# Optimization experiments

Measured on AMD Instinct MI355X. Metric: run time of the kernel, lower is better.

Reference implementation:

```python
import jax, jax.numpy as jnp
import numpy as np
import math

NH = 12  # num_attention_heads (multiple of 4 required by pattern dispatch)


def _forward(Input, hidden_states, attention_mask, Wq, bq, Wk, bk, Wv, bv, Wo, bo, L):
    b, n, _, H = Input.shape
    hd = H // NH
    G = NH // 4  # heads per criss-cross pattern
    # boolean-mask gather of valid (head, tail) entity pairs, row-major like torch
    bi, ri, ci = jnp.nonzero(attention_mask > 0, size=L)
    x = Input[bi, ri, ci]            # [L, H] keys/values source
    xq = hidden_states[bi, ri, ci]   # [L, H] query source
    q = (xq @ Wq + bq).reshape(L, NH, hd)
    k = (x @ Wk + bk).reshape(L, NH, hd)
    v = (x @ Wv + bv).reshape(L, NH, hd)
    ar = jnp.arange(n)
    # per-pattern criss-cross masks for query position (b, r, c), each [L, n]
    m0 = attention_mask[bi, ri, :] * (ar[None, :] != ci[:, None])  # row r, exclude self col c
    m1 = attention_mask[bi, :, ci] * (ar[None, :] != ri[:, None])  # col c, exclude self row r
    m2 = attention_mask[bi, :, ri]                                  # col r (no self exclusion)
    m3 = attention_mask[bi, ci, :]                                  # row c (no self exclusion)
    adds = jnp.stack([(1.0 - m) * -10000.0 for m in (m0, m1, m2, m3)], axis=1)  # [L, 4, n]
    # scatter per-pattern head groups into zero grid, then criss-cross gather
    k_gs, v_gs = [], []
    for p in range(4):
        sk = jnp.zeros((b, n, n, G, hd), k.dtype).at[bi, ri, ci].set(k[:, p::4])
        sv = jnp.zeros((b, n, n, G, hd), v.dtype).at[bi, ri, ci].set(v[:, p::4])
        if p == 0:
            gk, gv = sk[bi, ri], sv[bi, ri]          # element [l,k] = grid[b, r, k]
        elif p == 1:
            gk, gv = sk[bi, :, ci], sv[bi, :, ci]    # grid[b, k, c]
        elif p == 2:
            gk, gv = sk[bi, :, ri], sv[bi, :, ri]    # grid[b, k, r]
        else:
            gk, gv = sk[bi, ci], sv[bi, ci]          # grid[b, c, k]
        k_gs.append(gk)
        v_gs.append(gv)
    kg = jnp.stack(k_gs, axis=1)  # [L, 4, n, G, hd]
    vg = jnp.stack(v_gs, axis=1)
    # head h = 4*g + p (k[:, p::4] picks heads p, p+4, p+8)
    kg = kg.transpose(0, 3, 1, 2, 4).reshape(L, NH, n, hd)
    vg = vg.transpose(0, 3, 1, 2, 4).reshape(L, NH, n, hd)
    amask = jnp.broadcast_to(adds[:, None, :, :], (L, G, 4, n)).reshape(L, NH, n)
    # prepend self key/value; NOTE: original code uses additive bias +1.0 (ones) for the self slot
    kf = jnp.concatenate([k[:, :, None, :], kg], axis=2)   # [L, NH, n+1, hd]
    vf = jnp.concatenate([v[:, :, None, :], vg], axis=2)
    amask = jnp.concatenate([jnp.ones((L, NH, 1), amask.dtype), amask], axis=-1)
    scores = jnp.einsum('lhd,lhkd->lhk', q, kf) / math.sqrt(hd) + amask
    probs = jax.nn.softmax(scores, axis=-1)  # dropout is identity in eval
    ctx = jnp.einsum('lhk,lhkd->lhd', probs, vf).reshape(L, H)
    return ctx @ Wo + bo


def setup_inputs() -> dict:
    key = jax.random.key(0)
    ks = jax.random.split(key, 8)
    b, n, H = 2, 40, 768
    Input = jax.random.normal(ks[0], (b, n, n, H), jnp.float32)
    hidden_states = jax.random.normal(ks[1], (b, n, n, H), jnp.float32)
    # all valid entity pairs except self pairs -> deterministic L
    attention_mask = (jnp.ones((b, n, n)) - jnp.eye(n)[None]).astype(jnp.float32)
    L = int(b * n * (n - 1))  # 3120
    std = 0.02
    Wq = std * jax.random.normal(ks[2], (H, H), jnp.float32)
    Wk = std * jax.random.normal(ks[3], (H, H), jnp.float32)
    Wv = std * jax.random.normal(ks[4], (H, H), jnp.float32)
    Wo = std * jax.random.normal(ks[5], (H, H), jnp.float32)
    bq = jnp.zeros((H,), jnp.float32)
    bk = jnp.zeros((H,), jnp.float32)
    bv = jnp.zeros((H,), jnp.float32)
    bo = jnp.zeros((H,), jnp.float32)
    return {"Input": Input, "hidden_states": hidden_states, "attention_mask": attention_mask,
            "Wq": Wq, "bq": bq, "Wk": Wk, "bk": bk, "Wv": Wv, "bv": bv, "Wo": Wo, "bo": bo, "L": L}


def reference(Input, hidden_states, attention_mask, Wq, bq, Wk, bk, Wv, bv, Wo, bo, L):
    return _forward(Input, hidden_states, attention_mask, Wq, bq, Wk, bk, Wv, bv, Wo, bo, L)
```

## Files before the change

### kernel.cpp

```cpp
#include <hip/hip_runtime.h>
#include <hip/hip_bf16.h>
#include <math.h>

#define NHEADS 12

typedef __attribute__((ext_vector_type(4))) float f32x4;
typedef __attribute__((ext_vector_type(8))) short bf16x8;

__device__ __forceinline__ unsigned short f2bf(float x) {
  __hip_bfloat16 h = __float2bfloat16(x);
  return *reinterpret_cast<unsigned short*>(&h);
}
__device__ __forceinline__ float bf2f(unsigned short u) {
  union { unsigned int i; float f; } c; c.i = ((unsigned int)u) << 16; return c.f;
}

__global__ __launch_bounds__(256) void prep(const float* __restrict__ mask, int total,
                                            int* __restrict__ pos2l, int* __restrict__ lidx,
                                            const float* __restrict__ bk, const float* __restrict__ bv,
                                            float* __restrict__ bkv,
                                            const float* __restrict__ W0, const float* __restrict__ W1,
                                            const float* __restrict__ W2, const float* __restrict__ W3,
                                            unsigned short* __restrict__ T0, unsigned short* __restrict__ T1,
                                            unsigned short* __restrict__ T2, unsigned short* __restrict__ T3,
                                            int H) {
  int nt32 = H / 32;
  int nw = nt32 * nt32 * 4;
  int bx = blockIdx.x;
  int t = threadIdx.x;
  if (bx < nw) {
    __shared__ float tile[32][33];
    int z = bx / (nt32 * nt32);
    int rem = bx - z * nt32 * nt32;
    int byy = rem / nt32;
    int bxx = rem - byy * nt32;
    const float* W = (z == 0) ? W0 : (z == 1) ? W1 : (z == 2) ? W2 : W3;
    unsigned short* T = (z == 0) ? T0 : (z == 1) ? T1 : (z == 2) ? T2 : T3;
    int k0 = byy * 32, n0 = bxx * 32;
    int kk = t >> 3, n4 = (t & 7) * 4;
    float4 v = *reinterpret_cast<const float4*>(W + (size_t)(k0 + kk) * H + n0 + n4);
    tile[n4 + 0][kk] = v.x; tile[n4 + 1][kk] = v.y; tile[n4 + 2][kk] = v.z; tile[n4 + 3][kk] = v.w;
    __syncthreads();
    int nn2 = t >> 3, k4 = (t & 7) * 4;
#pragma unroll
    for (int e = 0; e < 4; ++e)
      T[(size_t)(n0 + nn2) * H + k0 + k4 + e] = f2bf(tile[nn2][k4 + e]);
  } else {
    __shared__ int cnt[256];
    for (int i = t; i < H; i += 256) { bkv[i] = bk[i]; bkv[H + i] = bv[i]; }
    int per = (total + 255) >> 8;
    int begin = t * per;
    int end = begin + per; if (end > total) end = total;
    if (begin > total) begin = total;
    int c = 0;
    for (int i = begin; i < end; ++i) c += (mask[i] > 0.f) ? 1 : 0;
    cnt[t] = c;
    __syncthreads();
    for (int off = 1; off < 256; off <<= 1) {
      int vv = (t >= off) ? cnt[t - off] : 0;
      __syncthreads();
      cnt[t] += vv;
      __syncthreads();
    }
    int excl = cnt[t] - c;
    for (int i = begin; i < end; ++i) {
      if (mask[i] > 0.f) { pos2l[i] = excl; lidx[excl] = i; ++excl; }
      else pos2l[i] = -1;
    }
  }
}

__global__ __launch_bounds__(256) void gatherconv(const float* __restrict__ hidden,
                                                  const float* __restrict__ input,
                                                  const int* __restrict__ lidx,
                                                  unsigned short* __restrict__ Aq,
                                                  unsigned short* __restrict__ Akv,
                                                  int L, int H) {
  int i = blockIdx.x * 256 + threadIdx.x;
  int per = H / 8;
  if (i >= L * per) return;
  int row = i / per;
  int sub = (i - row * per) * 8;
  size_t src = (size_t)lidx[row] * H + sub;
  size_t dst = (size_t)row * H + sub;
  {
    float4 a = *reinterpret_cast<const float4*>(hidden + src);
    float4 b = *reinterpret_cast<const float4*>(hidden + src + 4);
    bf16x8 st;
    st[0]=f2bf(a.x); st[1]=f2bf(a.y); st[2]=f2bf(a.z); st[3]=f2bf(a.w);
    st[4]=f2bf(b.x); st[5]=f2bf(b.y); st[6]=f2bf(b.z); st[7]=f2bf(b.w);
    *reinterpret_cast<bf16x8*>(Aq + dst) = st;
  }
  {
    float4 a = *reinterpret_cast<const float4*>(input + src);
    float4 b = *reinterpret_cast<const float4*>(input + src + 4);
    bf16x8 st;
    st[0]=f2bf(a.x); st[1]=f2bf(a.y); st[2]=f2bf(a.z); st[3]=f2bf(a.w);
    st[4]=f2bf(b.x); st[5]=f2bf(b.y); st[6]=f2bf(b.z); st[7]=f2bf(b.w);
    *reinterpret_cast<bf16x8*>(Akv + dst) = st;
  }
}

#define GBM 128
#define GBN 64
#define GBK 64

template <bool OUT_BF16>
__device__ __forceinline__ void gemm_core(const unsigned short* __restrict__ A,
                                          const unsigned short* __restrict__ Bt,
                                          const float* __restrict__ bias,
                                          void* __restrict__ C,
                                          int M, int N, int K, int m0, int n0,
                                          unsigned short* sA, unsigned short* sB) {
  int tid = threadIdx.x;
  int wid = tid >> 6, lane = tid & 63;
  int wm = wid >> 1, wn = wid & 1;
  int lr = lane & 15, lq = lane >> 4;
  f32x4 acc[4][2] = {};

  auto STAGE = [&](int buf, int k0) {
#pragma unroll
    for (int r = 0; r < 4; ++r) {
      int c = (r * 4 + wid) * 64 + lane;
      int row = c >> 3, sl = c & 7;
      int sg = sl ^ (row & 7);
      const unsigned short* g = A + (size_t)(m0 + row) * K + k0 + sg * 8;
      __builtin_amdgcn_global_load_lds((const __attribute__((address_space(1))) unsigned int*)g,
                                       (__attribute__((address_space(3))) unsigned int*)(sA + buf * (GBM * GBK) + (r * 4 + wid) * 512),
                                       16, 0, 0);
    }
#pragma unroll
    for (int r = 0; r < 2; ++r) {
      int c = (r * 4 + wid) * 64 + lane;
      int row = c >> 3, sl = c & 7;
      int sg = sl ^ (row & 7);
      const unsigned short* g = Bt + (size_t)(n0 + row) * K + k0 + sg * 8;
      __builtin_amdgcn_global_load_lds((const __attribute__((address_space(1))) unsigned int*)g,
                                       (__attribute__((address_space(3))) unsigned int*)(sB + buf * (GBN * GBK) + (r * 4 + wid) * 512),
                                       16, 0, 0);
    }
  };

  const int nt = K / GBK;
  STAGE(0, 0);
  int cur = 0;
  for (int t = 0; t < nt; ++t) {
    __syncthreads();
    if (t + 1 < nt) STAGE(cur ^ 1, (t + 1) * GBK);
    const unsigned short* pA = sA + cur * (GBM * GBK);
    const unsigned short* pB = sB + cur * (GBN * GBK);
#pragma unroll
    for (int ks = 0; ks < 2; ++ks) {
      bf16x8 af[4], bfr[2];
#pragma unroll
      for (int i = 0; i < 4; ++i) {
        int row = wm * 64 + i * 16 + lr;
        int slot = (ks * 4 + lq) ^ (row & 7);
        af[i] = *reinterpret_cast<const bf16x8*>(pA + row * 64 + slot * 8);
      }
#pragma unroll
      for (int j = 0; j < 2; ++j) {
        int rn = wn * 32 + j * 16 + lr;
        int slot = (ks * 4 + lq) ^ (rn & 7);
        bfr[j] = *reinterpret_cast<const bf16x8*>(pB + rn * 64 + slot * 8);
      }
#pragma unroll
      for (int i = 0; i < 4; ++i)
#pragma unroll
        for (int j = 0; j < 2; ++j)
          acc[i][j] = __builtin_amdgcn_mfma_f32_16x16x32_bf16(af[i], bfr[j], acc[i][j], 0, 0, 0);
    }
    cur ^= 1;
  }

#pragma unroll
  for (int i = 0; i < 4; ++i) {
#pragma unroll
    for (int j = 0; j < 2; ++j) {
      int gcol = n0 + wn * 32 + j * 16 + lr;
      float bv = bias[gcol];
      int rbase = m0 + wm * 64 + i * 16 + lq * 4;
#pragma unroll
      for (int r = 0; r < 4; ++r) {
        int gm = rbase + r;
        if (gm >= M) continue;
        float val = acc[i][j][r] + bv;
        if (OUT_BF16) ((unsigned short*)C)[(size_t)gm * N + gcol] = f2bf(val);
        else          ((float*)C)[(size_t)gm * N + gcol] = val;
      }
    }
  }
}

__global__ __launch_bounds__(256) void gemm_qkv(const unsigned short* __restrict__ Aq,
                                                const unsigned short* __restrict__ Akv,
                                                const unsigned short* __restrict__ Wqt,
                                                const unsigned short* __restrict__ Wkvt,
                                                const float* __restrict__ bq,
                                                const float* __restrict__ bkv,
                                                unsigned short* __restrict__ Cq,
                                                unsigned short* __restrict__ Ckv,
                                                int M, int K, int H) {
  __shared__ unsigned short sA[2 * GBM * GBK];
  __shared__ unsigned short sB[2 * GBN * GBK];
  int nq = H / GBN;
  int bx = blockIdx.x;
  int m0 = blockIdx.y * GBM;
  if (bx < nq)
    gemm_core<true>(Aq, Wqt, bq, Cq, M, H, K, m0, bx * GBN, sA, sB);
  else
    gemm_core<true>(Akv, Wkvt, bkv, Ckv, M, 2 * H, K, m0, (bx - nq) * GBN, sA, sB);
}

__global__ __launch_bounds__(256) void gemm_out(const unsigned short* __restrict__ A,
                                                const unsigned short* __restrict__ Bt,
                                                const float* __restrict__ bias,
                                                float* __restrict__ C,
                                                int M, int N, int K) {
  __shared__ unsigned short sA[2 * GBM * GBK];
  __shared__ unsigned short sB[2 * GBN * GBK];
  gemm_core<false>(A, Bt, bias, C, M, N, K, blockIdx.y * GBM, blockIdx.x * GBN, sA, sB);
}

__global__ __launch_bounds__(128) void attn3(const unsigned short* __restrict__ qb,
                                             const unsigned short* __restrict__ KVb,
                                             const float* __restrict__ mask,
                                             const int* __restrict__ pos2l,
                                             unsigned short* __restrict__ ctx,
                                             int n, int H) {
  __shared__ unsigned short Ks[40 * 72];
  __shared__ unsigned short Vs[40 * 72];
  __shared__ float S[40][42];
  __shared__ float mrow[40];
  __shared__ int qlist[40];

  int bx = blockIdx.x;
  int r0 = bx % n;
  int h3 = (bx / n) % 3;
  int p = (bx / (3 * n)) % 4;
  int bi = bx / (12 * n);
  int h = p + 4 * h3;
  int nn = n * n;
  bool rowkeys = (p == 0 || p == 3);
  bool rowq = (p == 0 || p == 2);
  bool excl = (p < 2);
  int t = threadIdx.x;
  int H2 = 2 * H;

  if (t < 80) {
    int half = t / 40, j = t % 40;
    int keypos = rowkeys ? (r0 * n + j) : (j * n + r0);
    int l2 = pos2l[bi * nn + keypos];
    unsigned short* dst = (half ? Vs : Ks) + j * 72;
    if (l2 >= 0) {
      const unsigned short* src = KVb + (size_t)l2 * H2 + half * H + h * 64;
#pragma unroll
      for (int e8 = 0; e8 < 8; ++e8)
        *reinterpret_cast<bf16x8*>(dst + e8 * 8) = *reinterpret_cast<const bf16x8*>(src + e8 * 8);
    } else {
      bf16x8 z = {};
#pragma unroll
      for (int e8 = 0; e8 < 8; ++e8) *reinterpret_cast<bf16x8*>(dst + e8 * 8) = z;
    }
  }
  if (t < 40) {
    mrow[t] = rowkeys ? mask[bi * nn + r0 * n + t] : mask[bi * nn + t * n + r0];
    int qpos = rowq ? (r0 * n + t) : (t * n + r0);
    qlist[t] = pos2l[bi * nn + qpos];
  }
  __syncthreads();

  int c = t % 40;
  int role = t / 40;
  int lq = (t < 80) ? qlist[c] : -1;

  if (lq >= 0) {
    float qf[64];
    const unsigned short* qp = qb + (size_t)lq * H + h * 64;
#pragma unroll
    for (int e8 = 0; e8 < 8; ++e8) {
      bf16x8 t8 = *reinterpret_cast<const bf16x8*>(qp + e8 * 8);
#pragma unroll
      for (int e = 0; e < 8; ++e) qf[e8 * 8 + e] = bf2f((unsigned short)t8[e]);
    }
    int j0 = role * 20;
#pragma unroll 2
    for (int j = j0; j < j0 + 20; ++j) {
      float acc = 0.f;
#pragma unroll
      for (int e8 = 0; e8 < 8; ++e8) {
        bf16x8 kv = *reinterpret_cast<const bf16x8*>(Ks + j * 72 + e8 * 8);
#pragma unroll
        for (int e = 0; e < 8; ++e) acc = fmaf(qf[e8 * 8 + e], bf2f((unsigned short)kv[e]), acc);
      }
      float mval = mrow[j] * ((excl && j == c) ? 0.f : 1.f);
      S[c][j] = acc * 0.125f + (1.f - mval) * -10000.f;
    }
    if (role == 0) {
      const unsigned short* kp = KVb + (size_t)lq * H2 + h * 64;
      float acc = 0.f;
#pragma unroll
      for (int e8 = 0; e8 < 8; ++e8) {
        bf16x8 kv = *reinterpret_cast<const bf16x8*>(kp + e8 * 8);
#pragma unroll
        for (int e = 0; e < 8; ++e) acc = fmaf(qf[e8 * 8 + e], bf2f((unsigned short)kv[e]), acc);
      }
      S[c][40] = acc * 0.125f + 1.0f;
    }
  }
  __syncthreads();

  if (t < 40 && qlist[t] >= 0) {
    float mx = -3.0e38f;
    for (int j = 0; j <= 40; ++j) mx = fmaxf(mx, S[t][j]);
    float sum = 0.f;
    for (int j = 0; j <= 40; ++j) { float e = __expf(S[t][j] - mx); S[t][j] = e; sum += e; }
    float inv = 1.f / sum;
    for (int j = 0; j <= 40; ++j) S[t][j] *= inv;
  }
  __syncthreads();

  if (lq >= 0) {
    int d0 = role * 32;
    const unsigned short* vsp = KVb + (size_t)lq * H2 + H + h * 64 + d0;
    float pself = S[c][40];
#pragma unroll
    for (int ch = 0; ch < 4; ++ch) {
      int dd = d0 + ch * 8;
      float facc[8];
      bf16x8 vself = *reinterpret_cast<const bf16x8*>(vsp + ch * 8);
#pragma unroll
      for (int e = 0; e < 8; ++e) facc[e] = pself * bf2f((unsigned short)vself[e]);
      for (int j = 0; j < 40; ++j) {
        float pj = S[c][j];
        bf16x8 vv = *reinterpret_cast<const bf16x8*>(Vs + j * 72 + dd);
#pragma unroll
        for (int e = 0; e < 8; ++e) facc[e] = fmaf(pj, bf2f((unsigned short)vv[e]), facc[e]);
      }
      bf16x8 st;
#pragma unroll
      for (int e = 0; e < 8; ++e) st[e] = f2bf(facc[e]);
      *reinterpret_cast<bf16x8*>(ctx + (size_t)lq * H + h * 64 + dd) = st;
    }
  }
}

extern "C" void kernel_launch(void* const* d_in, const int* in_sizes, int n_in,
                              void* d_out, int out_size, void* d_ws, size_t ws_size,
                              hipStream_t stream) {
  const float* Input  = (const float*)d_in[0];
  const float* hidden = (const float*)d_in[1];
  const float* mask   = (const float*)d_in[2];
  const float* Wq = (const float*)d_in[3];
  const float* bq = (const float*)d_in[4];
  const float* Wk = (const float*)d_in[5];
  const float* bk = (const float*)d_in[6];
  const float* Wv = (const float*)d_in[7];
  const float* bv = (const float*)d_in[8];
  const float* Wo = (const float*)d_in[9];
  const float* bo = (const float*)d_in[10];

  int H = (int)llround(sqrt((double)in_sizes[3]));
  int total = in_sizes[2];
  int L = out_size / H;
  int bn = total - L;
  int n = total / bn;
  int b = bn / n;
  int mtiles = (L + GBM - 1) / GBM;
  int Mpad = mtiles * GBM;
  size_t aElems = (size_t)Mpad * H;

  char* p = (char*)d_ws;
  auto take = [&](size_t bytes) { char* r = p; p += (bytes + 255) & ~(size_t)255; return r; };
  int* lidx  = (int*)take((size_t)L * 4);
  int* pos2l = (int*)take((size_t)total * 4);
  float* bkv = (float*)take((size_t)2 * H * 4);
  unsigned short* Wqt  = (unsigned short*)take((size_t)H * H * 2);
  unsigned short* Wot  = (unsigned short*)take((size_t)H * H * 2);
  unsigned short* Wkvt = (unsigned short*)take((size_t)2 * H * H * 2);
  unsigned short* Aq   = (unsigned short*)take(aElems * 2);
  unsigned short* Akv  = (unsigned short*)take(aElems * 2);
  unsigned short* qb2  = (unsigned short*)take(aElems * 2);
  unsigned short* KVb  = (unsigned short*)take(aElems * 2 * 2);
  unsigned short* ctxb = (unsigned short*)take(aElems * 2);

  int nt32 = H / 32;
  int nwconv = nt32 * nt32 * 4;
  prep<<<nwconv + 1, 256, 0, stream>>>(mask, total, pos2l, lidx, bk, bv, bkv,
                                       Wq, Wk, Wv, Wo,
                                       Wqt, Wkvt, Wkvt + (size_t)H * H, Wot, H);
  {
    int nthr = L * (H / 8);
    gatherconv<<<(nthr + 255) / 256, 256, 0, stream>>>(hidden, Input, lidx, Aq, Akv, L, H);
  }
  gemm_qkv<<<dim3(3 * H / GBN, mtiles), 256, 0, stream>>>(Aq, Akv, Wqt, Wkvt, bq, bkv,
                                                          qb2, KVb, L, H, H);
  attn3<<<b * 4 * 3 * n, 128, 0, stream>>>(qb2, KVb, mask, pos2l, ctxb, n, H);
  gemm_out<<<dim3(H / GBN, mtiles), 256, 0, stream>>>(ctxb, Wot, bo, (float*)d_out, L, H, H);
}
```

Before: 99.35 us.

## Widen QKV GEMM tile to 128x128 and drop LDS double buffering

The QKV projection GEMM now uses a 128x128 output tile, so each wave computes a 4x4 grid of MFMA fragments, and the grid has half as many column blocks. Both GEMMs drop the double-buffered LDS staging in favour of a single buffer guarded by two barriers per K step, and the output GEMM is inlined as its own kernel. The larger tile reuses each loaded A tile across more columns and the smaller LDS footprint may allow more resident blocks. The cost is that global loads no longer overlap with MFMA work, and the QKV grid is smaller (18x25 blocks), which may underfill the GPU.

```diff
diff --git a/kernel.cpp b/kernel.cpp
--- a/kernel.cpp
+++ b/kernel.cpp
@@ -101,83 +101,72 @@
   }
 }
 
-#define GBM 128
-#define GBN 64
-#define GBK 64
+#define QBM 128
+#define QBN 128
+#define QBK 64
 
 template <bool OUT_BF16>
-__device__ __forceinline__ void gemm_core(const unsigned short* __restrict__ A,
-                                          const unsigned short* __restrict__ Bt,
-                                          const float* __restrict__ bias,
-                                          void* __restrict__ C,
-                                          int M, int N, int K, int m0, int n0,
-                                          unsigned short* sA, unsigned short* sB) {
+__device__ __forceinline__ void gemm128_core(const unsigned short* __restrict__ A,
+                                             const unsigned short* __restrict__ Bt,
+                                             const float* __restrict__ bias,
+                                             void* __restrict__ C,
+                                             int M, int N, int K, int m0, int n0,
+                                             unsigned short* sA, unsigned short* sB) {
   int tid = threadIdx.x;
   int wid = tid >> 6, lane = tid & 63;
   int wm = wid >> 1, wn = wid & 1;
   int lr = lane & 15, lq = lane >> 4;
-  f32x4 acc[4][2] = {};
-
-  auto STAGE = [&](int buf, int k0) {
+  f32x4 acc[4][4] = {};
+
+  for (int k0 = 0; k0 < K; k0 += QBK) {
 #pragma unroll
     for (int r = 0; r < 4; ++r) {
       int c = (r * 4 + wid) * 64 + lane;
       int row = c >> 3, sl = c & 7;
       int sg = sl ^ (row & 7);
-      const unsigned short* g = A + (size_t)(m0 + row) * K + k0 + sg * 8;
-      __builtin_amdgcn_global_load_lds((const __attribute__((address_space(1))) unsigned int*)g,
-                                       (__attribute__((address_space(3))) unsigned int*)(sA + buf * (GBM * GBK) + (r * 4 + wid) * 512),
+      __builtin_amdgcn_global_load_lds((const __attribute__((address_space(1))) unsigned int*)(A + (size_t)(m0 + row) * K + k0 + sg * 8),
+                                       (__attribute__((address_space(3))) unsigned int*)(sA + (r * 4 + wid) * 512),
                                        16, 0, 0);
     }
 #pragma unroll
-    for (int r = 0; r < 2; ++r) {
+    for (int r = 0; r < 4; ++r) {
       int c = (r * 4 + wid) * 64 + lane;
       int row = c >> 3, sl = c & 7;
       int sg = sl ^ (row & 7);
-      const unsigned short* g = Bt + (size_t)(n0 + row) * K + k0 + sg * 8;
-      __builtin_amdgcn_global_load_lds((const __attribute__((address_space(1))) unsigned int*)g,
-                                       (__attribute__((address_space(3))) unsigned int*)(sB + buf * (GBN * GBK) + (r * 4 + wid) * 512),
+      __builtin_amdgcn_global_load_lds((const __attribute__((address_space(1))) unsigned int*)(Bt + (size_t)(n0 + row) * K + k0 + sg * 8),
+                                       (__attribute__((address_space(3))) unsigned int*)(sB + (r * 4 + wid) * 512),
                                        16, 0, 0);
     }
-  };
-
-  const int nt = K / GBK;
-  STAGE(0, 0);
-  int cur = 0;
-  for (int t = 0; t < nt; ++t) {
-    __syncthreads();
-    if (t + 1 < nt) STAGE(cur ^ 1, (t + 1) * GBK);
-    const unsigned short* pA = sA + cur * (GBM * GBK);
-    const unsigned short* pB = sB + cur * (GBN * GBK);
+    __syncthreads();
 #pragma unroll
     for (int ks = 0; ks < 2; ++ks) {
-      bf16x8 af[4], bfr[2];
+      bf16x8 af[4], bfr[4];
 #pragma unroll
       for (int i = 0; i < 4; ++i) {
         int row = wm * 64 + i * 16 + lr;
         int slot = (ks * 4 + lq) ^ (row & 7);
-        af[i] = *reinterpret_cast<const bf16x8*>(pA + row * 64 + slot * 8);
-      }
-#pragma unroll
-      for (int j = 0; j < 2; ++j) {
-        int rn = wn * 32 + j * 16 + lr;
+        af[i] = *reinterpret_cast<const bf16x8*>(sA + row * 64 + slot * 8);
+      }
+#pragma unroll
+      for (int j = 0; j < 4; ++j) {
+        int rn = wn * 64 + j * 16 + lr;
         int slot = (ks * 4 + lq) ^ (rn & 7);
-        bfr[j] = *reinterpret_cast<const bf16x8*>(pB + rn * 64 + slot * 8);
+        bfr[j] = *reinterpret_cast<const bf16x8*>(sB + rn * 64 + slot * 8);
       }
 #pragma unroll
       for (int i = 0; i < 4; ++i)
 #pragma unroll
-        for (int j = 0; j < 2; ++j)
+        for (int j = 0; j < 4; ++j)
           acc[i][j] = __builtin_amdgcn_mfma_f32_16x16x32_bf16(af[i], bfr[j], acc[i][j], 0, 0, 0);
     }
-    cur ^= 1;
+    __syncthreads();
   }
 
 #pragma unroll
   for (int i = 0; i < 4; ++i) {
 #pragma unroll
-    for (int j = 0; j < 2; ++j) {
-      int gcol = n0 + wn * 32 + j * 16 + lr;
+    for (int j = 0; j < 4; ++j) {
+      int gcol = n0 + wn * 64 + j * 16 + lr;
       float bv = bias[gcol];
       int rbase = m0 + wm * 64 + i * 16 + lq * 4;
 #pragma unroll
@@ -201,25 +190,94 @@
                                                 unsigned short* __restrict__ Cq,
                                                 unsigned short* __restrict__ Ckv,
                                                 int M, int K, int H) {
-  __shared__ unsigned short sA[2 * GBM * GBK];
-  __shared__ unsigned short sB[2 * GBN * GBK];
-  int nq = H / GBN;
+  __shared__ unsigned short sA[QBM * QBK];
+  __shared__ unsigned short sB[QBN * QBK];
+  int nq = H / QBN;
   int bx = blockIdx.x;
-  int m0 = blockIdx.y * GBM;
+  int m0 = blockIdx.y * QBM;
   if (bx < nq)
-    gemm_core<true>(Aq, Wqt, bq, Cq, M, H, K, m0, bx * GBN, sA, sB);
+    gemm128_core<true>(Aq, Wqt, bq, Cq, M, H, K, m0, bx * QBN, sA, sB);
   else
-    gemm_core<true>(Akv, Wkvt, bkv, Ckv, M, 2 * H, K, m0, (bx - nq) * GBN, sA, sB);
-}
+    gemm128_core<true>(Akv, Wkvt, bkv, Ckv, M, 2 * H, K, m0, (bx - nq) * QBN, sA, sB);
+}
+
+#define GBM 128
+#define GBN 64
+#define GBK 64
 
 __global__ __launch_bounds__(256) void gemm_out(const unsigned short* __restrict__ A,
                                                 const unsigned short* __restrict__ Bt,
                                                 const float* __restrict__ bias,
                                                 float* __restrict__ C,
                                                 int M, int N, int K) {
-  __shared__ unsigned short sA[2 * GBM * GBK];
-  __shared__ unsigned short sB[2 * GBN * GBK];
-  gemm_core<false>(A, Bt, bias, C, M, N, K, blockIdx.y * GBM, blockIdx.x * GBN, sA, sB);
+  __shared__ unsigned short sA[GBM * GBK];
+  __shared__ unsigned short sB[GBN * GBK];
+  int tid = threadIdx.x;
+  int wid = tid >> 6, lane = tid & 63;
+  int wm = wid >> 1, wn = wid & 1;
+  int m0 = blockIdx.y * GBM, n0 = blockIdx.x * GBN;
+  int lr = lane & 15, lq = lane >> 4;
+  f32x4 acc[4][2] = {};
+
+  for (int k0 = 0; k0 < K; k0 += GBK) {
+#pragma unroll
+    for (int r = 0; r < 4; ++r) {
+      int c = (r * 4 + wid) * 64 + lane;
+      int row = c >> 3, sl = c & 7;
+      int sg = sl ^ (row & 7);
+      __builtin_amdgcn_global_load_lds((const __attribute__((address_space(1))) unsigned int*)(A + (size_t)(m0 + row) * K + k0 + sg * 8),
+                                       (__attribute__((address_space(3))) unsigned int*)(sA + (r * 4 + wid) * 512),
+                                       16, 0, 0);
+    }
+#pragma unroll
+    for (int r = 0; r < 2; ++r) {
+      int c = (r * 4 + wid) * 64 + lane;
+      int row = c >> 3, sl = c & 7;
+      int sg = sl ^ (row & 7);
+      __builtin_amdgcn_global_load_lds((const __attribute__((address_space(1))) unsigned int*)(Bt + (size_t)(n0 + row) * K + k0 + sg * 8),
+                                       (__attribute__((address_space(3))) unsigned int*)(sB + (r * 4 + wid) * 512),
+                                       16, 0, 0);
+    }
+    __syncthreads();
+#pragma unroll
+    for (int ks = 0; ks < 2; ++ks) {
+      bf16x8 af[4], bfr[2];
+#pragma unroll
+      for (int i = 0; i < 4; ++i) {
+        int row = wm * 64 + i * 16 + lr;
+        int slot = (ks * 4 + lq) ^ (row & 7);
+        af[i] = *reinterpret_cast<const bf16x8*>(sA + row * 64 + slot * 8);
+      }
+#pragma unroll
+      for (int j = 0; j < 2; ++j) {
+        int rn = wn * 32 + j * 16 + lr;
+        int slot = (ks * 4 + lq) ^ (rn & 7);
+        bfr[j] = *reinterpret_cast<const bf16x8*>(sB + rn * 64 + slot * 8);
+      }
+#pragma unroll
+      for (int i = 0; i < 4; ++i)
+#pragma unroll
+        for (int j = 0; j < 2; ++j)
+          acc[i][j] = __builtin_amdgcn_mfma_f32_16x16x32_bf16(af[i], bfr[j], acc[i][j], 0, 0, 0);
+    }
+    __syncthreads();
+  }
+
+#pragma unroll
+  for (int i = 0; i < 4; ++i) {
+#pragma unroll
+    for (int j = 0; j < 2; ++j) {
+      int gcol = n0 + wn * 32 + j * 16 + lr;
+      float bv = bias[gcol];
+      int rbase = m0 + wm * 64 + i * 16 + lq * 4;
+#pragma unroll
+      for (int r = 0; r < 4; ++r) {
+        int gm = rbase + r;
+        if (gm >= M) continue;
+        C[(size_t)gm * N + gcol] = acc[i][j][r] + bv;
+      }
+    }
+  }
 }
 
 __global__ __launch_bounds__(128) void attn3(const unsigned short* __restrict__ qb,
@@ -366,8 +424,8 @@
   int bn = total - L;
   int n = total / bn;
   int b = bn / n;
-  int mtiles = (L + GBM - 1) / GBM;
-  int Mpad = mtiles * GBM;
+  int mtiles = (L + QBM - 1) / QBM;
+  int Mpad = mtiles * QBM;
   size_t aElems = (size_t)Mpad * H;
 
   char* p = (char*)d_ws;
@@ -393,7 +451,7 @@
     int nthr = L * (H / 8);
     gatherconv<<<(nthr + 255) / 256, 256, 0, stream>>>(hidden, Input, lidx, Aq, Akv, L, H);
   }
-  gemm_qkv<<<dim3(3 * H / GBN, mtiles), 256, 0, stream>>>(Aq, Akv, Wqt, Wkvt, bq, bkv,
+  gemm_qkv<<<dim3(3 * H / QBN, mtiles), 256, 0, stream>>>(Aq, Akv, Wqt, Wkvt, bq, bkv,
                                                           qb2, KVb, L, H, H);
   attn3<<<b * 4 * 3 * n, 128, 0, stream>>>(qb2, KVb, mask, pos2l, ctxb, n, H);
   gemm_out<<<dim3(H / GBN, mtiles), 256, 0, stream>>>(ctxb, Wot, bo, (float*)d_out, L, H, H);
```

After: 88.26 us. 11.2% less time.
